# Performance work log

Measured on AMD Instinct MI355X. Metric: run time of the kernel, lower is better.

Reference implementation:

```python
import jax, jax.numpy as jnp
import numpy as np

# physics constants (match init_kwargs)
DT = 1.0 / 60.0
G_ACC = 9.81
RHO = 1.225
CD = 0.47
NU = 0.001
B, N, GRID = 512, 64, 16


def _norm(x):
    return jnp.linalg.norm(x, axis=-1, keepdims=True)


def _deriv(pos, vel, rot, omega, mass, inertia, contacts, fluid_v,
           Fext, tau, log_A, log_k, log_b, conv_w):
    g_vec = jnp.array([0.0, 0.0, -G_ACC], dtype=pos.dtype)
    Fg = mass[..., None] * g_vec                                  # [B,N,3]
    A = jax.nn.softplus(log_A).reshape(1, -1, 1)
    vm = jnp.maximum(_norm(vel), 1e-6)
    Fd = -0.5 * RHO * CD * A * vm * vel                           # drag
    k = jax.nn.softplus(log_k)
    b = jax.nn.softplus(log_b)
    d_ij = pos[:, None, :, :] - pos[:, :, None, :]                # [B,N,N,3] = p_j - p_i
    dist = jnp.maximum(_norm(d_ij), 1e-6)
    n_hat = d_ij / dist
    pen = jax.nn.relu(1.0 - dist[..., 0])                         # penetration depth
    dvel = vel[:, None, :, :] - vel[:, :, None, :]                # v_j - v_i
    Fc = (k * pen[..., None] * n_hat + b * dvel * contacts[..., None]).sum(axis=2)
    dv = (Fext + Fg + Fd + Fc) / mass[..., None]
    Io = inertia * omega
    domega = (tau - jnp.cross(omega, Io)) / jnp.maximum(inertia, 1e-6)
    w, x, y, z = rot[..., 0], rot[..., 1], rot[..., 2], rot[..., 3]
    ox, oy, oz = omega[..., 0], omega[..., 1], omega[..., 2]
    drot = 0.5 * jnp.stack([
        -x * ox - y * oy - z * oz,
        w * ox + y * oz - z * oy,
        w * oy - x * oz + z * ox,
        w * oz + x * oy - y * ox], axis=-1)
    P_in = (Fext * vel).sum((-1, -2))
    P_dis = -(Fd * vel).sum((-1, -2))
    dE = P_in - P_dis
    Bsz = fluid_v.shape[0]
    u = fluid_v.reshape(Bsz, GRID, GRID, GRID, 3).transpose(0, 4, 1, 2, 3)  # NCDHW
    dfluid = NU * jax.lax.conv_general_dilated(
        u, conv_w, window_strides=(1, 1, 1), padding=[(1, 1)] * 3,
        feature_group_count=3,
        dimension_numbers=('NCDHW', 'OIDHW', 'NCDHW'))
    dfluid = dfluid.transpose(0, 2, 3, 4, 1).reshape(Bsz, GRID ** 3, 3)
    return vel, dv, drot, domega, dE, dfluid


def _quat_normalize(q):
    return q / jnp.maximum(_norm(q), 1e-12)


def _apply(pos, vel, rot, omega, fluid_v, dt, dp, dv, dr, dw, dfluid):
    npos = pos + dt * dp
    nvel = vel + dt * dv
    nrot = _quat_normalize(rot + dt * dr)
    nomega = omega + dt * dw
    new_u = fluid_v + dt * dfluid
    nfluid = new_u - new_u.mean(axis=1, keepdims=True)
    return npos, nvel, nrot, nomega, nfluid


def _forward(pos, vel, rot, omega, mass, inertia, contacts, energy, fluid_v,
             Fext, tau, log_A, log_k, log_b, conv_w):
    dt = DT
    params = (mass, inertia, contacts)

    def deriv(p, v, r, o, fv):
        return _deriv(p, v, r, o, mass, inertia, contacts, fv,
                      Fext, tau, log_A, log_k, log_b, conv_w)

    k1 = deriv(pos, vel, rot, omega, fluid_v)
    s2 = _apply(pos, vel, rot, omega, fluid_v, dt / 2, k1[0], k1[1], k1[2], k1[3], k1[5])
    k2 = deriv(*s2)
    s3 = _apply(pos, vel, rot, omega, fluid_v, dt / 2, k2[0], k2[1], k2[2], k2[3], k2[5])
    k3 = deriv(*s3)
    s4 = _apply(pos, vel, rot, omega, fluid_v, dt, k3[0], k3[1], k3[2], k3[3], k3[5])
    k4 = deriv(*s4)

    def rk4c(y, a, b_, c, d):
        return y + dt / 6 * (a + 2 * b_ + 2 * c + d)

    npos = rk4c(pos, k1[0], k2[0], k3[0], k4[0])
    nvel = rk4c(vel, k1[1], k2[1], k3[1], k4[1])
    nrot = _quat_normalize(rk4c(rot, k1[2], k2[2], k3[2], k4[2]))
    nomega = rk4c(omega, k1[3], k2[3], k3[3], k4[3])
    nenergy = rk4c(energy, k1[4], k2[4], k3[4], k4[4])
    nforces = Fext + mass[..., None] * k1[1]
    raw_fluid = rk4c(fluid_v, k1[5], k2[5], k3[5], k4[5])
    nfluid = raw_fluid - raw_fluid.mean(axis=1, keepdims=True)
    Bsz = pos.shape[0]
    # flatten new state: [pos, vel, rot, omega, forces, energy, fluid_v]
    return jnp.concatenate([
        npos.reshape(Bsz, -1), nvel.reshape(Bsz, -1), nrot.reshape(Bsz, -1),
        nomega.reshape(Bsz, -1), nforces.reshape(Bsz, -1),
        nenergy[:, None], nfluid.reshape(Bsz, -1)], axis=-1)


def setup_inputs() -> dict:
    key = jax.random.key(0)
    ks = jax.random.split(key, 12)
    rot = jax.random.normal(ks[2], (B, N, 4), dtype=jnp.float32)
    rot = rot / jnp.maximum(jnp.linalg.norm(rot, axis=-1, keepdims=True), 1e-12)
    return {
        'pos': 2.0 * jax.random.normal(ks[0], (B, N, 3), dtype=jnp.float32),
        'vel': jax.random.normal(ks[1], (B, N, 3), dtype=jnp.float32),
        'rot': rot,
        'omega': jax.random.normal(ks[3], (B, N, 3), dtype=jnp.float32),
        'mass': 0.5 + jax.random.uniform(ks[4], (B, N), dtype=jnp.float32),
        'inertia': 0.05 + 0.1 * jax.random.uniform(ks[5], (B, N, 3), dtype=jnp.float32),
        'contacts': jax.random.uniform(ks[6], (B, N, N), dtype=jnp.float32),
        'energy': jnp.zeros((B,), dtype=jnp.float32),
        'fluid_v': jax.random.normal(ks[7], (B, GRID ** 3, 3), dtype=jnp.float32),
        'Fext': jax.random.normal(ks[8], (B, N, 3), dtype=jnp.float32),
        'tau': jax.random.normal(ks[9], (B, N, 3), dtype=jnp.float32),
        'log_A': jnp.zeros((N,), dtype=jnp.float32),
        'log_k': jnp.full((1,), np.log(1000.0), dtype=jnp.float32),
        'log_b': jnp.full((1,), np.log(10.0), dtype=jnp.float32),
        'conv_w': 0.1 * jax.random.normal(ks[10], (3, 1, 3, 3, 3), dtype=jnp.float32),
    }


def reference(pos, vel, rot, omega, mass, inertia, contacts, energy, fluid_v,
              Fext, tau, log_A, log_k, log_b, conv_w):
    return _forward(pos, vel, rot, omega, mass, inertia, contacts, energy,
                    fluid_v, Fext, tau, log_A, log_k, log_b, conv_w)
```

## Files before the change

### kernel.cpp

```cpp
#include <hip/hip_runtime.h>

#define DT (1.0f/60.0f)
#define G_ACC 9.81f
#define RHO 1.225f
#define CD_ 0.47f
#define NU 0.001f

__device__ __forceinline__ float softplus_f(float x) {
    return log1pf(expf(-fabsf(x))) + fmaxf(x, 0.0f);
}

#define RL(v, l) __int_as_float(__builtin_amdgcn_readlane(__float_as_int(v), (l)))

__device__ __forceinline__ float dpp_xm(float v) {
    return __int_as_float(__builtin_amdgcn_update_dpp(0, __float_as_int(v), 0x111, 0xf, 0xf, true));
}
__device__ __forceinline__ float dpp_xp(float v) {
    return __int_as_float(__builtin_amdgcn_update_dpp(0, __float_as_int(v), 0x101, 0xf, 0xf, true));
}

__global__ __launch_bounds__(256) void fused_kernel(
    const float* __restrict__ pos, const float* __restrict__ vel,
    const float* __restrict__ rot, const float* __restrict__ omega,
    const float* __restrict__ mass, const float* __restrict__ inertia,
    const float* __restrict__ contacts, const float* __restrict__ energy,
    const float* __restrict__ fluid, const float* __restrict__ Fext,
    const float* __restrict__ tau, const float* __restrict__ log_A,
    const float* __restrict__ log_k, const float* __restrict__ log_b,
    const float* __restrict__ conv_w, float* __restrict__ out)
{
    __shared__ float smem[4384];
    const int t = threadIdx.x;

    if (blockIdx.x < 1536) {
        const int b  = blockIdx.x & 511;
        const int ch = blockIdx.x >> 9;
        const int x  = t & 15, y = t >> 4, wv = t >> 6;
        float* u   = smem;
        float* wch = smem + 4352;
        float* red = smem + 4380;
        if (t < 27) wch[t] = conv_w[ch*27 + t];

        const int lb = t*17;
        const float* fb = fluid + (size_t)b*12288 + 3*t + ch;
        float base[16], acc[16];
        #pragma unroll
        for (int z = 0; z < 16; ++z) {
            float v = fb[z*768];
            base[z] = v; acc[z] = 0.f; u[lb + z] = v;
        }
        __syncthreads();

        const float mm = (y > 0)  ? 1.f : 0.f;
        const float pm = (y < 15) ? 1.f : 0.f;
        const float xm = (x > 0)  ? 1.f : 0.f;
        const float xp = (x < 15) ? 1.f : 0.f;
        const int   cm = (y > 0)  ? lb - 272 : lb;
        const int   cp = (y < 15) ? lb + 272 : lb;

        float Sdz[3];
        #pragma unroll
        for (int dz = 0; dz < 3; ++dz) {
            float a0 = wch[dz*9+0]*xm + wch[dz*9+1] + wch[dz*9+2]*xp;
            float a1 = wch[dz*9+3]*xm + wch[dz*9+4] + wch[dz*9+5]*xp;
            float a2 = wch[dz*9+6]*xm + wch[dz*9+7] + wch[dz*9+8]*xp;
            Sdz[dz] = mm*a0 + a1 + pm*a2;
        }
        const float SzLo  = Sdz[1] + Sdz[2];
        const float SzMid = Sdz[0] + Sdz[1] + Sdz[2];
        const float SzHi  = Sdz[0] + Sdz[1];
        const float* W = wch + 0;

        const float wgt[4] = {1.f, 2.f, 2.f, 1.f};
        const float hs[3]  = {DT*0.5f, DT*0.5f, DT};
        float mean = 0.f;

        #define ACC3(c, wi) { \
            float w0_ = W[wi], w1_ = W[9+(wi)], w2_ = W[18+(wi)]; \
            _Pragma("unroll") for (int z = 0; z < 16; ++z) o[z] += w1_ * (c)[z]; \
            _Pragma("unroll") for (int z = 1; z < 16; ++z) o[z] += w0_ * (c)[z-1]; \
            _Pragma("unroll") for (int z = 0; z < 15; ++z) o[z] += w2_ * (c)[z+1]; }

        for (int s = 0; s < 4; ++s) {
            float o[16];
            #pragma unroll
            for (int z = 0; z < 16; ++z) o[z] = 0.f;

            {
                float c0[16], cl[16], cr[16];
                #pragma unroll
                for (int z = 0; z < 16; ++z) c0[z] = u[lb + z];
                #pragma unroll
                for (int z = 0; z < 16; ++z) { cl[z] = dpp_xm(c0[z]); cr[z] = dpp_xp(c0[z]); }
                ACC3(c0, 4); ACC3(cl, 3); ACC3(cr, 5);
            }
            {
                float c0[16], cl[16], cr[16];
                #pragma unroll
                for (int z = 0; z < 16; ++z) c0[z] = u[cm + z] * mm;
                #pragma unroll
                for (int z = 0; z < 16; ++z) { cl[z] = dpp_xm(c0[z]); cr[z] = dpp_xp(c0[z]); }
                ACC3(c0, 1); ACC3(cl, 0); ACC3(cr, 2);
            }
            {
                float c0[16], cl[16], cr[16];
                #pragma unroll
                for (int z = 0; z < 16; ++z) c0[z] = u[cp + z] * pm;
                #pragma unroll
                for (int z = 0; z < 16; ++z) { cl[z] = dpp_xm(c0[z]); cr[z] = dpp_xp(c0[z]); }
                ACC3(c0, 7); ACC3(cl, 6); ACC3(cr, 8);
            }

            float w = wgt[s];
            if (s < 3) {
                float h = hs[s], ps = 0.f, wn[16];
                #pragma unroll
                for (int z = 0; z < 16; ++z) {
                    float Sz = (z == 0) ? SzLo : ((z == 15) ? SzHi : SzMid);
                    float k = NU * (o[z] - mean * Sz);
                    acc[z] += w * k;
                    wn[z] = base[z] + h * k;
                    ps += wn[z];
                }
                #pragma unroll
                for (int off = 32; off > 0; off >>= 1) ps += __shfl_xor(ps, off, 64);
                __syncthreads();
                #pragma unroll
                for (int z = 0; z < 16; ++z) u[lb + z] = wn[z];
                if ((t & 63) == 0) red[wv] = ps;
                __syncthreads();
                mean = (red[0] + red[1] + red[2] + red[3]) * (1.0f/4096.0f);
            } else {
                #pragma unroll
                for (int z = 0; z < 16; ++z) {
                    float Sz = (z == 0) ? SzLo : ((z == 15) ? SzHi : SzMid);
                    acc[z] += w * NU * (o[z] - mean * Sz);
                }
            }
        }
        #undef ACC3

        float raw[16], ps = 0.f;
        #pragma unroll
        for (int z = 0; z < 16; ++z) { raw[z] = base[z] + (DT/6.0f)*acc[z]; ps += raw[z]; }
        #pragma unroll
        for (int off = 32; off > 0; off >>= 1) ps += __shfl_xor(ps, off, 64);
        __syncthreads();
        if ((t & 63) == 0) red[wv] = ps;
        __syncthreads();
        float mn = (red[0] + red[1] + red[2] + red[3]) * (1.0f/4096.0f);

        float* ob = out + (size_t)b*13313 + 1025 + 3*t + ch;
        #pragma unroll
        for (int z = 0; z < 16; ++z) ob[z*768] = raw[z] - mn;
        return;
    }

    const int b = blockIdx.x - 1536;
    const int q = t >> 6;
    const int i = t & 63;
    #define SF(buf, qq, idx) smem[(buf)*768 + (qq)*192 + (idx)]

    const float* cbase = contacts + (size_t)b*4096 + (size_t)i*64 + q*16;
    float4 cA = ((const float4*)cbase)[0];
    float4 cB = ((const float4*)cbase)[1];
    float4 cC = ((const float4*)cbase)[2];
    float4 cD = ((const float4*)cbase)[3];
    float cj[16] = {cA.x,cA.y,cA.z,cA.w, cB.x,cB.y,cB.z,cB.w,
                    cC.x,cC.y,cC.z,cC.w, cD.x,cD.y,cD.z,cD.w};

    const size_t p3 = ((size_t)b*64 + i)*3;
    const size_t p4 = ((size_t)b*64 + i)*4;
    float bpx=pos[p3],   bpy=pos[p3+1],   bpz=pos[p3+2];
    float bvx=vel[p3],   bvy=vel[p3+1],   bvz=vel[p3+2];
    float brw=rot[p4],   brx=rot[p4+1],   bry=rot[p4+2],  brz=rot[p4+3];
    float box=omega[p3], boy=omega[p3+1], boz=omega[p3+2];
    float m  = mass[(size_t)b*64+i];
    float Ix=inertia[p3], Iy=inertia[p3+1], Iz=inertia[p3+2];
    float Fex=Fext[p3],   Fey=Fext[p3+1],   Fez=Fext[p3+2];
    float tx=tau[p3],     ty=tau[p3+1],     tz=tau[p3+2];
    float Ai = softplus_f(log_A[i]);
    float kc = softplus_f(log_k[0]);
    float bc = softplus_f(log_b[0]);
    float dragc = -0.5f * RHO * CD_ * Ai;
    float invm  = 1.0f / m;
    float iIx = 1.0f/fmaxf(Ix,1e-6f), iIy = 1.0f/fmaxf(Iy,1e-6f), iIz = 1.0f/fmaxf(Iz,1e-6f);

    float cpx=bpx, cpy=bpy, cpz=bpz;
    float cvx=bvx, cvy=bvy, cvz=bvz;
    float crw=brw, crx=brx, cry=bry, crz=brz;
    float cox=box, coy=boy, coz=boz;

    float apx=0,apy=0,apz=0, avx=0,avy=0,avz=0;
    float arw=0,arx=0,ary=0,arz=0, awx=0,awy=0,awz=0;
    float eacc=0.f;
    float k1vx=0,k1vy=0,k1vz=0;

    const float wgt[4] = {1.f, 2.f, 2.f, 1.f};
    const float hs[4]  = {DT*0.5f, DT*0.5f, DT, 0.f};
    const int j0 = q << 4;

    for (int s = 0; s < 4; ++s) {
        float Fcx=0.f, Fcy=0.f, Fcz=0.f;
        #pragma unroll
        for (int jj = 0; jj < 16; ++jj) {
            const int j = j0 + jj;
            float pjx = RL(cpx, j), pjy = RL(cpy, j), pjz = RL(cpz, j);
            float vjx = RL(cvx, j), vjy = RL(cvy, j), vjz = RL(cvz, j);
            float dx = pjx - cpx, dy = pjy - cpy, dz = pjz - cpz;
            float d2 = dx*dx + dy*dy + dz*dz;
            float dist = fmaxf(sqrtf(d2), 1e-6f);
            float pen  = fmaxf(1.0f - dist, 0.0f);
            float coef = kc * pen * __builtin_amdgcn_rcpf(dist);
            float cbj  = bc * cj[jj];
            Fcx += coef*dx + cbj*(vjx - cvx);
            Fcy += coef*dy + cbj*(vjy - cvy);
            Fcz += coef*dz + cbj*(vjz - cvz);
        }
        const int buf = s & 1;
        SF(buf, q, i*3+0) = Fcx;
        SF(buf, q, i*3+1) = Fcy;
        SF(buf, q, i*3+2) = Fcz;
        __syncthreads();
        Fcx = SF(buf,0,i*3+0) + SF(buf,1,i*3+0) + SF(buf,2,i*3+0) + SF(buf,3,i*3+0);
        Fcy = SF(buf,0,i*3+1) + SF(buf,1,i*3+1) + SF(buf,2,i*3+1) + SF(buf,3,i*3+1);
        Fcz = SF(buf,0,i*3+2) + SF(buf,1,i*3+2) + SF(buf,2,i*3+2) + SF(buf,3,i*3+2);

        float vm = fmaxf(sqrtf(cvx*cvx+cvy*cvy+cvz*cvz), 1e-6f);
        float dc = dragc * vm;
        float Fdx = dc*cvx, Fdy = dc*cvy, Fdz = dc*cvz;

        float dvx = (Fex + Fdx + Fcx) * invm;
        float dvy = (Fey + Fdy + Fcy) * invm;
        float dvz = (Fez - m*G_ACC + Fdz + Fcz) * invm;

        float dqw = 0.5f*(-crx*cox - cry*coy - crz*coz);
        float dqx = 0.5f*( crw*cox + cry*coz - crz*coy);
        float dqy = 0.5f*( crw*coy - crx*coz + crz*cox);
        float dqz = 0.5f*( crw*coz + crx*coy - cry*cox);

        float Iox = Ix*cox, Ioy = Iy*coy, Ioz = Iz*coz;
        float cxv = coy*Ioz - coz*Ioy;
        float cyv = coz*Iox - cox*Ioz;
        float czv = cox*Ioy - coy*Iox;
        float dwx = (tx - cxv) * iIx;
        float dwy = (ty - cyv) * iIy;
        float dwz = (tz - czv) * iIz;

        float ei = (Fex+Fdx)*cvx + (Fey+Fdy)*cvy + (Fez+Fdz)*cvz;
        #pragma unroll
        for (int off = 32; off > 0; off >>= 1) ei += __shfl_xor(ei, off, 64);

        float w = wgt[s];
        eacc += w * ei;
        if (s == 0) { k1vx=dvx; k1vy=dvy; k1vz=dvz; }
        apx += w*cvx; apy += w*cvy; apz += w*cvz;
        avx += w*dvx; avy += w*dvy; avz += w*dvz;
        arw += w*dqw; arx += w*dqx; ary += w*dqy; arz += w*dqz;
        awx += w*dwx; awy += w*dwy; awz += w*dwz;

        if (s < 3) {
            float h = hs[s];
            float npx = bpx + h*cvx, npy = bpy + h*cvy, npz = bpz + h*cvz;
            cvx = bvx + h*dvx; cvy = bvy + h*dvy; cvz = bvz + h*dvz;
            cpx = npx; cpy = npy; cpz = npz;
            float qw = brw + h*dqw, qx = brx + h*dqx, qy = bry + h*dqy, qz = brz + h*dqz;
            float iqn = 1.0f / fmaxf(sqrtf(qw*qw+qx*qx+qy*qy+qz*qz), 1e-12f);
            crw = qw*iqn; crx = qx*iqn; cry = qy*iqn; crz = qz*iqn;
            cox = box + h*dwx; coy = boy + h*dwy; coz = boz + h*dwz;
        }
    }

    if (q == 0) {
        const float s6 = DT / 6.0f;
        float* ob = out + (size_t)b * 13313;
        ob[      i*3+0] = bpx + s6*apx;  ob[      i*3+1] = bpy + s6*apy;  ob[      i*3+2] = bpz + s6*apz;
        ob[192 + i*3+0] = bvx + s6*avx;  ob[192 + i*3+1] = bvy + s6*avy;  ob[192 + i*3+2] = bvz + s6*avz;
        {
            float qw=brw+s6*arw, qx=brx+s6*arx, qy=bry+s6*ary, qz=brz+s6*arz;
            float iq = 1.0f / fmaxf(sqrtf(qw*qw+qx*qx+qy*qy+qz*qz), 1e-12f);
            ob[384 + i*4+0]=qw*iq; ob[384 + i*4+1]=qx*iq; ob[384 + i*4+2]=qy*iq; ob[384 + i*4+3]=qz*iq;
        }
        ob[640 + i*3+0] = box + s6*awx;  ob[640 + i*3+1] = boy + s6*awy;  ob[640 + i*3+2] = boz + s6*awz;
        ob[832 + i*3+0] = Fex + m*k1vx;  ob[832 + i*3+1] = Fey + m*k1vy;  ob[832 + i*3+2] = Fez + m*k1vz;
        if (i == 0) ob[1024] = energy[b] + s6*eacc;
    }
    #undef SF
}

extern "C" void kernel_launch(void* const* d_in, const int* in_sizes, int n_in,
                              void* d_out, int out_size, void* d_ws, size_t ws_size,
                              hipStream_t stream) {
    const float* pos      = (const float*)d_in[0];
    const float* vel      = (const float*)d_in[1];
    const float* rot      = (const float*)d_in[2];
    const float* omega    = (const float*)d_in[3];
    const float* mass     = (const float*)d_in[4];
    const float* inertia  = (const float*)d_in[5];
    const float* contacts = (const float*)d_in[6];
    const float* energy   = (const float*)d_in[7];
    const float* fluid_v  = (const float*)d_in[8];
    const float* Fext     = (const float*)d_in[9];
    const float* tau      = (const float*)d_in[10];
    const float* log_A    = (const float*)d_in[11];
    const float* log_k    = (const float*)d_in[12];
    const float* log_b    = (const float*)d_in[13];
    const float* conv_w   = (const float*)d_in[14];
    float* out = (float*)d_out;

    fused_kernel<<<dim3(2048), dim3(256), 0, stream>>>(
        pos, vel, rot, omega, mass, inertia, contacts, energy, fluid_v,
        Fext, tau, log_A, log_k, log_b, conv_w, out);
}
```

Before: 158.7 us.

## Cut register pressure in fused fluid and contact kernel for higher occupancy

The fluid stencil now streams each z-plane through a single pass, so it no longer holds three 16-wide neighbour arrays, and the zero-padding row for the y boundaries comes from a zeroed shared-memory pad. Conv weights are pre-scaled by NU and kept in scalar registers. The contact path stages the contacts matrix in padded shared memory rather than registers and drops the double-buffered force reduction in favour of an extra barrier. The launch bound asks for 8 waves per SIMD so that more blocks run at once. The extra syncs and larger shared-memory footprint could offset the occupancy gain, and the forced register cap could cause spills.

```diff
diff --git a/kernel.cpp b/kernel.cpp
--- a/kernel.cpp
+++ b/kernel.cpp
@@ -11,6 +11,7 @@
 }
 
 #define RL(v, l) __int_as_float(__builtin_amdgcn_readlane(__float_as_int(v), (l)))
+#define SLANE(x) __int_as_float(__builtin_amdgcn_readfirstlane(__float_as_int(x)))
 
 __device__ __forceinline__ float dpp_xm(float v) {
     return __int_as_float(__builtin_amdgcn_update_dpp(0, __float_as_int(v), 0x111, 0xf, 0xf, true));
@@ -19,7 +20,7 @@
     return __int_as_float(__builtin_amdgcn_update_dpp(0, __float_as_int(v), 0x101, 0xf, 0xf, true));
 }
 
-__global__ __launch_bounds__(256) void fused_kernel(
+__global__ __launch_bounds__(256, 8) void fused_kernel(
     const float* __restrict__ pos, const float* __restrict__ vel,
     const float* __restrict__ rot, const float* __restrict__ omega,
     const float* __restrict__ mass, const float* __restrict__ inertia,
@@ -29,7 +30,7 @@
     const float* __restrict__ log_k, const float* __restrict__ log_b,
     const float* __restrict__ conv_w, float* __restrict__ out)
 {
-    __shared__ float smem[4384];
+    __shared__ float smem[4928];
     const int t = threadIdx.x;
 
     if (blockIdx.x < 1536) {
@@ -37,9 +38,12 @@
         const int ch = blockIdx.x >> 9;
         const int x  = t & 15, y = t >> 4, wv = t >> 6;
         float* u   = smem;
-        float* wch = smem + 4352;
-        float* red = smem + 4380;
-        if (t < 27) wch[t] = conv_w[ch*27 + t];
+        float* red = smem + 4368;
+        if (t < 16) smem[4352 + t] = 0.f;
+
+        float W[27];
+        #pragma unroll
+        for (int k = 0; k < 27; ++k) W[k] = NU * SLANE(conv_w[ch*27 + k]);
 
         const int lb = t*17;
         const float* fb = fluid + (size_t)b*12288 + 3*t + ch;
@@ -49,84 +53,67 @@
             float v = fb[z*768];
             base[z] = v; acc[z] = 0.f; u[lb + z] = v;
         }
+
+        const float xm = (x > 0) ? 1.f : 0.f, xp = (x < 15) ? 1.f : 0.f;
+        const float mm = (y > 0) ? 1.f : 0.f, pm = (y < 15) ? 1.f : 0.f;
+        float Sdz0, Sdz1, Sdz2;
+        {
+            float a0 = W[0]*xm + W[1] + W[2]*xp;
+            float a1 = W[3]*xm + W[4] + W[5]*xp;
+            float a2 = W[6]*xm + W[7] + W[8]*xp;
+            Sdz0 = mm*a0 + a1 + pm*a2;
+            a0 = W[ 9]*xm + W[10] + W[11]*xp;
+            a1 = W[12]*xm + W[13] + W[14]*xp;
+            a2 = W[15]*xm + W[16] + W[17]*xp;
+            Sdz1 = mm*a0 + a1 + pm*a2;
+            a0 = W[18]*xm + W[19] + W[20]*xp;
+            a1 = W[21]*xm + W[22] + W[23]*xp;
+            a2 = W[24]*xm + W[25] + W[26]*xp;
+            Sdz2 = mm*a0 + a1 + pm*a2;
+        }
+        const float SzLo = Sdz1 + Sdz2, SzHi = Sdz0 + Sdz1, SzMid = Sdz0 + Sdz1 + Sdz2;
+        const int cm = (y > 0)  ? lb - 272 : 4352;
+        const int cp = (y < 15) ? lb + 272 : 4352;
+
         __syncthreads();
-
-        const float mm = (y > 0)  ? 1.f : 0.f;
-        const float pm = (y < 15) ? 1.f : 0.f;
-        const float xm = (x > 0)  ? 1.f : 0.f;
-        const float xp = (x < 15) ? 1.f : 0.f;
-        const int   cm = (y > 0)  ? lb - 272 : lb;
-        const int   cp = (y < 15) ? lb + 272 : lb;
-
-        float Sdz[3];
-        #pragma unroll
-        for (int dz = 0; dz < 3; ++dz) {
-            float a0 = wch[dz*9+0]*xm + wch[dz*9+1] + wch[dz*9+2]*xp;
-            float a1 = wch[dz*9+3]*xm + wch[dz*9+4] + wch[dz*9+5]*xp;
-            float a2 = wch[dz*9+6]*xm + wch[dz*9+7] + wch[dz*9+8]*xp;
-            Sdz[dz] = mm*a0 + a1 + pm*a2;
-        }
-        const float SzLo  = Sdz[1] + Sdz[2];
-        const float SzMid = Sdz[0] + Sdz[1] + Sdz[2];
-        const float SzHi  = Sdz[0] + Sdz[1];
-        const float* W = wch + 0;
-
-        const float wgt[4] = {1.f, 2.f, 2.f, 1.f};
-        const float hs[3]  = {DT*0.5f, DT*0.5f, DT};
         float mean = 0.f;
 
-        #define ACC3(c, wi) { \
-            float w0_ = W[wi], w1_ = W[9+(wi)], w2_ = W[18+(wi)]; \
-            _Pragma("unroll") for (int z = 0; z < 16; ++z) o[z] += w1_ * (c)[z]; \
-            _Pragma("unroll") for (int z = 1; z < 16; ++z) o[z] += w0_ * (c)[z-1]; \
-            _Pragma("unroll") for (int z = 0; z < 15; ++z) o[z] += w2_ * (c)[z+1]; }
-
+        #define SEC(ca, dy) { \
+            _Pragma("unroll") \
+            for (int z = 0; z < 16; ++z) { \
+                float c  = u[(ca) + z]; \
+                float cl = dpp_xm(c), cr = dpp_xp(c); \
+                o[z] += W[9+(dy)*3+1]*c + W[9+(dy)*3]*cl + W[9+(dy)*3+2]*cr; \
+                if (z < 15) o[z+1] += W[(dy)*3+1]*c + W[(dy)*3]*cl + W[(dy)*3+2]*cr; \
+                if (z > 0)  o[z-1] += W[18+(dy)*3+1]*c + W[18+(dy)*3]*cl + W[18+(dy)*3+2]*cr; \
+            } }
+
+        #pragma unroll
         for (int s = 0; s < 4; ++s) {
             float o[16];
             #pragma unroll
             for (int z = 0; z < 16; ++z) o[z] = 0.f;
-
-            {
-                float c0[16], cl[16], cr[16];
-                #pragma unroll
-                for (int z = 0; z < 16; ++z) c0[z] = u[lb + z];
-                #pragma unroll
-                for (int z = 0; z < 16; ++z) { cl[z] = dpp_xm(c0[z]); cr[z] = dpp_xp(c0[z]); }
-                ACC3(c0, 4); ACC3(cl, 3); ACC3(cr, 5);
-            }
-            {
-                float c0[16], cl[16], cr[16];
-                #pragma unroll
-                for (int z = 0; z < 16; ++z) c0[z] = u[cm + z] * mm;
-                #pragma unroll
-                for (int z = 0; z < 16; ++z) { cl[z] = dpp_xm(c0[z]); cr[z] = dpp_xp(c0[z]); }
-                ACC3(c0, 1); ACC3(cl, 0); ACC3(cr, 2);
-            }
-            {
-                float c0[16], cl[16], cr[16];
-                #pragma unroll
-                for (int z = 0; z < 16; ++z) c0[z] = u[cp + z] * pm;
-                #pragma unroll
-                for (int z = 0; z < 16; ++z) { cl[z] = dpp_xm(c0[z]); cr[z] = dpp_xp(c0[z]); }
-                ACC3(c0, 7); ACC3(cl, 6); ACC3(cr, 8);
-            }
-
-            float w = wgt[s];
+            SEC(lb, 1);
+            SEC(cm, 0);
+            SEC(cp, 2);
+
             if (s < 3) {
-                float h = hs[s], ps = 0.f, wn[16];
+                const float h = (s == 2) ? DT : DT*0.5f;
+                const float w = (s == 0) ? 1.f : 2.f;
+                float ps = 0.f;
                 #pragma unroll
                 for (int z = 0; z < 16; ++z) {
                     float Sz = (z == 0) ? SzLo : ((z == 15) ? SzHi : SzMid);
-                    float k = NU * (o[z] - mean * Sz);
+                    float k = o[z] - mean * Sz;
                     acc[z] += w * k;
-                    wn[z] = base[z] + h * k;
-                    ps += wn[z];
+                    float v = base[z] + h * k;
+                    o[z] = v; ps += v;
                 }
                 #pragma unroll
                 for (int off = 32; off > 0; off >>= 1) ps += __shfl_xor(ps, off, 64);
                 __syncthreads();
                 #pragma unroll
-                for (int z = 0; z < 16; ++z) u[lb + z] = wn[z];
+                for (int z = 0; z < 16; ++z) u[lb + z] = o[z];
                 if ((t & 63) == 0) red[wv] = ps;
                 __syncthreads();
                 mean = (red[0] + red[1] + red[2] + red[3]) * (1.0f/4096.0f);
@@ -134,40 +121,46 @@
                 #pragma unroll
                 for (int z = 0; z < 16; ++z) {
                     float Sz = (z == 0) ? SzLo : ((z == 15) ? SzHi : SzMid);
-                    acc[z] += w * NU * (o[z] - mean * Sz);
+                    acc[z] += o[z] - mean * Sz;
                 }
             }
         }
-        #undef ACC3
-
-        float raw[16], ps = 0.f;
-        #pragma unroll
-        for (int z = 0; z < 16; ++z) { raw[z] = base[z] + (DT/6.0f)*acc[z]; ps += raw[z]; }
+        #undef SEC
+
+        float ps = 0.f;
+        float o[16];
+        #pragma unroll
+        for (int z = 0; z < 16; ++z) { o[z] = base[z] + (DT/6.0f)*acc[z]; ps += o[z]; }
         #pragma unroll
         for (int off = 32; off > 0; off >>= 1) ps += __shfl_xor(ps, off, 64);
         __syncthreads();
         if ((t & 63) == 0) red[wv] = ps;
         __syncthreads();
-        float mn = (red[0] + red[1] + red[2] + red[3]) * (1.0f/4096.0f);
+        const float mn = (red[0] + red[1] + red[2] + red[3]) * (1.0f/4096.0f);
 
         float* ob = out + (size_t)b*13313 + 1025 + 3*t + ch;
         #pragma unroll
-        for (int z = 0; z < 16; ++z) ob[z*768] = raw[z] - mn;
+        for (int z = 0; z < 16; ++z) ob[z*768] = o[z] - mn;
         return;
     }
 
     const int b = blockIdx.x - 1536;
     const int q = t >> 6;
     const int i = t & 63;
-    #define SF(buf, qq, idx) smem[(buf)*768 + (qq)*192 + (idx)]
-
-    const float* cbase = contacts + (size_t)b*4096 + (size_t)i*64 + q*16;
-    float4 cA = ((const float4*)cbase)[0];
-    float4 cB = ((const float4*)cbase)[1];
-    float4 cC = ((const float4*)cbase)[2];
-    float4 cD = ((const float4*)cbase)[3];
-    float cj[16] = {cA.x,cA.y,cA.z,cA.w, cB.x,cB.y,cB.z,cB.w,
-                    cC.x,cC.y,cC.z,cC.w, cD.x,cD.y,cD.z,cD.w};
+    float* cont = smem;
+    float* sF   = smem + 4160;
+
+    {
+        const float4* cg = (const float4*)(contacts + (size_t)b*4096);
+        #pragma unroll
+        for (int v = 0; v < 4; ++v) {
+            float4 c4 = cg[v*256 + t];
+            int fi = (v*256 + t) * 4;
+            int r = fi >> 6, cc = fi & 63;
+            float* p = cont + r*65 + cc;
+            p[0] = c4.x; p[1] = c4.y; p[2] = c4.z; p[3] = c4.w;
+        }
+    }
 
     const size_t p3 = ((size_t)b*64 + i)*3;
     const size_t p4 = ((size_t)b*64 + i)*4;
@@ -179,11 +172,10 @@
     float Ix=inertia[p3], Iy=inertia[p3+1], Iz=inertia[p3+2];
     float Fex=Fext[p3],   Fey=Fext[p3+1],   Fez=Fext[p3+2];
     float tx=tau[p3],     ty=tau[p3+1],     tz=tau[p3+2];
-    float Ai = softplus_f(log_A[i]);
-    float kc = softplus_f(log_k[0]);
-    float bc = softplus_f(log_b[0]);
-    float dragc = -0.5f * RHO * CD_ * Ai;
-    float invm  = 1.0f / m;
+    float dragc = -0.5f * RHO * CD_ * softplus_f(log_A[i]);
+    float kc = softplus_f(SLANE(log_k[0]));
+    float bc = softplus_f(SLANE(log_b[0]));
+    float invm = 1.0f / m;
     float iIx = 1.0f/fmaxf(Ix,1e-6f), iIy = 1.0f/fmaxf(Iy,1e-6f), iIz = 1.0f/fmaxf(Iz,1e-6f);
 
     float cpx=bpx, cpy=bpy, cpz=bpz;
@@ -194,12 +186,12 @@
     float apx=0,apy=0,apz=0, avx=0,avy=0,avz=0;
     float arw=0,arx=0,ary=0,arz=0, awx=0,awy=0,awz=0;
     float eacc=0.f;
-    float k1vx=0,k1vy=0,k1vz=0;
-
-    const float wgt[4] = {1.f, 2.f, 2.f, 1.f};
-    const float hs[4]  = {DT*0.5f, DT*0.5f, DT, 0.f};
+
     const int j0 = q << 4;
-
+    float* ob = out + (size_t)b * 13313;
+    __syncthreads();
+
+    #pragma unroll
     for (int s = 0; s < 4; ++s) {
         float Fcx=0.f, Fcy=0.f, Fcz=0.f;
         #pragma unroll
@@ -208,23 +200,21 @@
             float pjx = RL(cpx, j), pjy = RL(cpy, j), pjz = RL(cpz, j);
             float vjx = RL(cvx, j), vjy = RL(cvy, j), vjz = RL(cvz, j);
             float dx = pjx - cpx, dy = pjy - cpy, dz = pjz - cpz;
-            float d2 = dx*dx + dy*dy + dz*dz;
-            float dist = fmaxf(sqrtf(d2), 1e-6f);
+            float dist = fmaxf(sqrtf(dx*dx + dy*dy + dz*dz), 1e-6f);
             float pen  = fmaxf(1.0f - dist, 0.0f);
             float coef = kc * pen * __builtin_amdgcn_rcpf(dist);
-            float cbj  = bc * cj[jj];
+            float cbj  = bc * cont[i*65 + j];
             Fcx += coef*dx + cbj*(vjx - cvx);
             Fcy += coef*dy + cbj*(vjy - cvy);
             Fcz += coef*dz + cbj*(vjz - cvz);
         }
-        const int buf = s & 1;
-        SF(buf, q, i*3+0) = Fcx;
-        SF(buf, q, i*3+1) = Fcy;
-        SF(buf, q, i*3+2) = Fcz;
+        sF[q*192 + i*3+0] = Fcx;
+        sF[q*192 + i*3+1] = Fcy;
+        sF[q*192 + i*3+2] = Fcz;
         __syncthreads();
-        Fcx = SF(buf,0,i*3+0) + SF(buf,1,i*3+0) + SF(buf,2,i*3+0) + SF(buf,3,i*3+0);
-        Fcy = SF(buf,0,i*3+1) + SF(buf,1,i*3+1) + SF(buf,2,i*3+1) + SF(buf,3,i*3+1);
-        Fcz = SF(buf,0,i*3+2) + SF(buf,1,i*3+2) + SF(buf,2,i*3+2) + SF(buf,3,i*3+2);
+        Fcx = sF[i*3+0] + sF[192+i*3+0] + sF[384+i*3+0] + sF[576+i*3+0];
+        Fcy = sF[i*3+1] + sF[192+i*3+1] + sF[384+i*3+1] + sF[576+i*3+1];
+        Fcz = sF[i*3+2] + sF[192+i*3+2] + sF[384+i*3+2] + sF[576+i*3+2];
 
         float vm = fmaxf(sqrtf(cvx*cvx+cvy*cvy+cvz*cvz), 1e-6f);
         float dc = dragc * vm;
@@ -233,6 +223,12 @@
         float dvx = (Fex + Fdx + Fcx) * invm;
         float dvy = (Fey + Fdy + Fcy) * invm;
         float dvz = (Fez - m*G_ACC + Fdz + Fcz) * invm;
+
+        if (s == 0 && q == 0) {
+            ob[832 + i*3+0] = Fex + m*dvx;
+            ob[832 + i*3+1] = Fey + m*dvy;
+            ob[832 + i*3+2] = Fez + m*dvz;
+        }
 
         float dqw = 0.5f*(-crx*cox - cry*coy - crz*coz);
         float dqx = 0.5f*( crw*cox + cry*coz - crz*coy);
@@ -240,27 +236,23 @@
         float dqz = 0.5f*( crw*coz + crx*coy - cry*cox);
 
         float Iox = Ix*cox, Ioy = Iy*coy, Ioz = Iz*coz;
-        float cxv = coy*Ioz - coz*Ioy;
-        float cyv = coz*Iox - cox*Ioz;
-        float czv = cox*Ioy - coy*Iox;
-        float dwx = (tx - cxv) * iIx;
-        float dwy = (ty - cyv) * iIy;
-        float dwz = (tz - czv) * iIz;
+        float dwx = (tx - (coy*Ioz - coz*Ioy)) * iIx;
+        float dwy = (ty - (coz*Iox - cox*Ioz)) * iIy;
+        float dwz = (tz - (cox*Ioy - coy*Iox)) * iIz;
 
         float ei = (Fex+Fdx)*cvx + (Fey+Fdy)*cvy + (Fez+Fdz)*cvz;
         #pragma unroll
         for (int off = 32; off > 0; off >>= 1) ei += __shfl_xor(ei, off, 64);
 
-        float w = wgt[s];
+        const float w = (s == 0 || s == 3) ? 1.f : 2.f;
         eacc += w * ei;
-        if (s == 0) { k1vx=dvx; k1vy=dvy; k1vz=dvz; }
         apx += w*cvx; apy += w*cvy; apz += w*cvz;
         avx += w*dvx; avy += w*dvy; avz += w*dvz;
         arw += w*dqw; arx += w*dqx; ary += w*dqy; arz += w*dqz;
         awx += w*dwx; awy += w*dwy; awz += w*dwz;
 
         if (s < 3) {
-            float h = hs[s];
+            const float h = (s == 2) ? DT : DT*0.5f;
             float npx = bpx + h*cvx, npy = bpy + h*cvy, npz = bpz + h*cvz;
             cvx = bvx + h*dvx; cvy = bvy + h*dvy; cvz = bvz + h*dvz;
             cpx = npx; cpy = npy; cpz = npz;
@@ -268,12 +260,12 @@
             float iqn = 1.0f / fmaxf(sqrtf(qw*qw+qx*qx+qy*qy+qz*qz), 1e-12f);
             crw = qw*iqn; crx = qx*iqn; cry = qy*iqn; crz = qz*iqn;
             cox = box + h*dwx; coy = boy + h*dwy; coz = boz + h*dwz;
+            __syncthreads();
         }
     }
 
     if (q == 0) {
         const float s6 = DT / 6.0f;
-        float* ob = out + (size_t)b * 13313;
         ob[      i*3+0] = bpx + s6*apx;  ob[      i*3+1] = bpy + s6*apy;  ob[      i*3+2] = bpz + s6*apz;
         ob[192 + i*3+0] = bvx + s6*avx;  ob[192 + i*3+1] = bvy + s6*avy;  ob[192 + i*3+2] = bvz + s6*avz;
         {
@@ -282,10 +274,8 @@
             ob[384 + i*4+0]=qw*iq; ob[384 + i*4+1]=qx*iq; ob[384 + i*4+2]=qy*iq; ob[384 + i*4+3]=qz*iq;
         }
         ob[640 + i*3+0] = box + s6*awx;  ob[640 + i*3+1] = boy + s6*awy;  ob[640 + i*3+2] = boz + s6*awz;
-        ob[832 + i*3+0] = Fex + m*k1vx;  ob[832 + i*3+1] = Fey + m*k1vy;  ob[832 + i*3+2] = Fez + m*k1vz;
         if (i == 0) ob[1024] = energy[b] + s6*eacc;
     }
-    #undef SF
 }
 
 extern "C" void kernel_launch(void* const* d_in, const int* in_sizes, int n_in,
```

After: 568.9 us. 3.58x slower.
